# Optimization experiments

Hardware: AMD Instinct MI355X
Metric: run time of the kernel (lower is better)

## Reference

```python
import jax, jax.numpy as jnp
import numpy as np

B, S, HID = 1, 4096, 1024
NH, HD = 16, 64            # heads, per-head dim
BS = 256                    # block size
PB = 256                    # position buckets (= max_relative_positions)
EPS = 1e-7


def make_log_bucket_position(rel, num_buckets, max_position):
    sign = jnp.sign(rel)
    max_exact = num_buckets // 2
    in_exact = (rel < max_exact) & (rel > -max_exact)
    abs_pos = jnp.where(in_exact, max_exact - 1, jnp.abs(rel))
    x = jnp.log((max_position - 1) / max_exact)
    xx = jnp.log(abs_pos / max_exact) / x
    log_pos = jnp.ceil(xx * (max_exact - 1)) + max_exact
    return jnp.where(abs_pos <= max_exact, rel, (log_pos * sign).astype(jnp.int32)).astype(jnp.int32)


def split_into_blocks(x, block_size, axis):
    # [..., S, ...] -> [..., S//bs, bs, ...]; S assumed divisible by bs
    shp = x.shape
    new = shp[:axis] + (shp[axis] // block_size, block_size) + shp[axis + 1:]
    return x.reshape(new)


def concat_3_blocks(x, block_axis, seq_axis, pad_value=0):
    # pad one zero block on each side of the block axis, then concat
    # [prev, cur, next] along the within-block seq axis.
    pad = [(0, 0)] * x.ndim
    pad[block_axis] = (1, 1)
    xp = jnp.pad(x, pad, constant_values=pad_value)
    nb = x.shape[block_axis]
    slices = [jax.lax.dynamic_slice_in_dim(xp, i, nb, block_axis) for i in range(3)]
    return jnp.concatenate(slices, axis=seq_axis)


def layer_norm(x, scale, bias):
    mu = jnp.mean(x, axis=-1, keepdims=True)
    var = jnp.mean(jnp.square(x - mu), axis=-1, keepdims=True)
    return (x - mu) * jax.lax.rsqrt(var + EPS) * scale + bias


def setup_inputs() -> dict:
    key = jax.random.key(0)
    ks = jax.random.split(key, 8)
    d = {
        'hidden_states': jax.random.normal(ks[0], (B, S, HID), jnp.float32) * 0.02,
        'rel_pos_embeddings': jax.random.normal(ks[1], (S, HID), jnp.float32) * 0.02,
        'Wq': jax.random.normal(ks[2], (HID, HID), jnp.float32) * 0.01,
        'bq': jnp.zeros((HID,), jnp.float32),
        'Wk': jax.random.normal(ks[3], (HID, HID), jnp.float32) * 0.01,
        'bk': jnp.zeros((HID,), jnp.float32),
        'Wv': jax.random.normal(ks[4], (HID, HID), jnp.float32) * 0.01,
        'bv': jnp.zeros((HID,), jnp.float32),
        'Wo': jax.random.normal(ks[5], (HID, HID), jnp.float32) * 0.01,
        'bo': jnp.zeros((HID,), jnp.float32),
        'ln_scale': jnp.ones((HID,), jnp.float32),
        'ln_bias': jnp.zeros((HID,), jnp.float32),
    }
    return d


def reference(hidden_states, rel_pos_embeddings, Wq, bq, Wk, bk, Wv, bv, Wo, bo, ln_scale, ln_bias):
    b, s, hid = hidden_states.shape

    def heads(x):
        return x.reshape(x.shape[:-1] + (NH, HD))

    # content projections -> [B, nb, bs, h, d]
    q = split_into_blocks(heads(hidden_states @ Wq + bq), BS, axis=1)
    k = split_into_blocks(heads(hidden_states @ Wk + bk), BS, axis=1)
    v = split_into_blocks(heads(hidden_states @ Wv + bv), BS, axis=1)
    k3 = concat_3_blocks(k, block_axis=1, seq_axis=2)   # [B, nb, 3bs, h, d]
    v3 = concat_3_blocks(v, block_axis=1, seq_axis=2)

    c2c = jnp.einsum('bnqhd,bnkhd->bnhqk', q, k3)

    # position projections, stacked over batch (size-1 batch dim broadcasts in einsum)
    pos_q = split_into_blocks(heads(rel_pos_embeddings @ Wq + bq)[None], BS, axis=1)  # [1, nb, bs, h, d]
    pos_k = split_into_blocks(heads(rel_pos_embeddings @ Wk + bk)[None], BS, axis=1)
    pos_k3 = concat_3_blocks(pos_k, block_axis=1, seq_axis=2)                          # [1, nb, 3bs, h, d]

    rel = jnp.arange(BS, dtype=jnp.int32)[:, None] - jnp.arange(3 * BS, dtype=jnp.int32)[None, :]
    rel = make_log_bucket_position(rel, PB, PB)
    idx = jnp.clip(rel + PB, 0, 2 * PB - 1)            # [bs, 3bs]

    c2p = jnp.einsum('bnqhd,bnkhd->bnhqk', q, pos_k3)  # [B, nb, h, bs, 3bs]
    # faithful to the source: axis-less jnp.take gathers from the FLATTENED
    # score tensor -> [bs, 3bs] bias broadcast over (batch, block, head)
    c2p_bias = jnp.take(c2p, idx)

    p2c = jnp.einsum('bnqhd,bnkhd->bnhqk', pos_q, k3)
    p2c_bias = jnp.take(p2c, idx)

    scale = jnp.sqrt(jnp.asarray(HD * 3, hidden_states.dtype))
    attn = (c2c + c2p_bias + p2c_bias) / scale
    probs = jax.nn.softmax(attn, axis=-1)

    ctx = jnp.einsum('bnhqk,bnkhd->bnqhd', probs, v3)  # [B, nb, bs, h, d]
    ctx = ctx.reshape(b, s, hid)
    out = ctx @ Wo + bo
    return layer_norm(out + hidden_states, ln_scale, ln_bias)
```

## Files before the change

### kernel.cpp

```cpp
#include <hip/hip_runtime.h>
#include <stdint.h>

typedef unsigned short u16;
typedef __bf16 bf16_t;
typedef bf16_t v8bf __attribute__((ext_vector_type(8)));
typedef float v4f __attribute__((ext_vector_type(4)));

#define SEQ   4096
#define HIDN  1024
#define NHEAD 16
#define HDIM  64
#define BLK   256
#define NBLK  16

#define GLOAD_LDS16(g, l) __builtin_amdgcn_global_load_lds( \
  (const __attribute__((address_space(1))) unsigned*)(g), \
  (__attribute__((address_space(3))) unsigned*)(l), 16, 0, 0)

__device__ __forceinline__ u16 f2bf(float f){
  union { float f; unsigned u; } v; v.f = f;
  unsigned r = (v.u + 0x7fffu + ((v.u >> 16) & 1u)) >> 16;
  return (u16)r;
}
__device__ __forceinline__ float bf2f(u16 h){
  union { unsigned u; float f; } v; v.u = ((unsigned)h) << 16;
  return v.f;
}

__global__ __launch_bounds__(256) void k_prep(const float* __restrict__ hidden, u16* __restrict__ hb,
    const float* __restrict__ Wq, const float* __restrict__ Wk,
    const float* __restrict__ Wv, const float* __restrict__ Wo, u16* __restrict__ Wt,
    const float* __restrict__ bq, const float* __restrict__ bk, const float* __restrict__ bv,
    float* __restrict__ bcat,
    const float* __restrict__ rpe, float* __restrict__ posk, float* __restrict__ posq0)
{
  __shared__ float t[32][33];
  __shared__ float red[4][64];
  int b = blockIdx.x, tid = threadIdx.x;
  if (b < 4096){
    int w = b >> 10, tile = b & 1023;
    int k0 = (tile & 31) * 32, n0 = (tile >> 5) * 32;
    const float* W = (w == 0) ? Wq : (w == 1) ? Wk : (w == 2) ? Wv : Wo;
    u16* outp = Wt + (size_t)w * 1024 * 1024;
    int x = tid & 31, y = tid >> 5;
    #pragma unroll
    for (int yy = 0; yy < 32; yy += 8) t[y + yy][x] = W[(size_t)(k0 + y + yy) * 1024 + n0 + x];
    __syncthreads();
    #pragma unroll
    for (int yy = 0; yy < 32; yy += 8) outp[(size_t)(n0 + y + yy) * 1024 + k0 + x] = f2bf(t[x][y + yy]);
  } else if (b < 4608){
    int base = (b - 4096) * 8192;
    #pragma unroll
    for (int j = 0; j < 8; j++){
      int i = base + j * 1024 + tid * 4;
      float4 f = *(const float4*)&hidden[i];
      unsigned u0 = (unsigned)f2bf(f.x) | ((unsigned)f2bf(f.y) << 16);
      unsigned u1 = (unsigned)f2bf(f.z) | ((unsigned)f2bf(f.w) << 16);
      uint2 p; p.x = u0; p.y = u1;
      *(uint2*)&hb[i] = p;
    }
  } else if (b == 4608){
    #pragma unroll
    for (int j = 0; j < 12; j++){
      int i = j * 256 + tid;
      const float* src = i < 1024 ? bq : (i < 2048 ? bk : bv);
      bcat[i] = src[i & 1023];
    }
  } else {
    int pb = b - 4609;
    int d = tid & 63, part = tid >> 6;
    const float* W  = (pb < 256) ? Wk : Wq;
    const float* rv = (pb < 256) ? &rpe[(size_t)pb * 1024] : rpe;
    float s = 0.f;
    for (int k = part * 256; k < part * 256 + 256; k++) s += rv[k] * W[(size_t)k * 1024 + d];
    red[part][d] = s;
    __syncthreads();
    if (part == 0){
      s = red[0][d] + red[1][d] + red[2][d] + red[3][d];
      if (pb < 256) posk[pb * 64 + d] = s + bk[d];
      else          posq0[d] = s + bq[d];
    }
  }
}

__global__ __launch_bounds__(256) void k_gemm_qkv(const u16* __restrict__ A, const u16* __restrict__ Bt,
                                                  const float* __restrict__ bias,
                                                  u16* __restrict__ qk, u16* __restrict__ Vt)
{
  __shared__ alignas(16) u16 As[128 * 32];
  __shared__ alignas(16) u16 Bs[128 * 32];
  int tid = threadIdx.x, lane = tid & 63, wid = tid >> 6;
  int wr = wid >> 1, wc = wid & 1;
  int m0 = blockIdx.y * 128, n0 = blockIdx.x * 128;
  const int K = 1024;

  v4f acc[4][4];
  #pragma unroll
  for (int m = 0; m < 4; m++)
    #pragma unroll
    for (int n = 0; n < 4; n++) acc[m][n] = (v4f){0.f, 0.f, 0.f, 0.f};

  int r = lane & 15, g = lane >> 4;
  int ob0 = wid * 2048;

  for (int kt = 0; kt < K; kt += 32){
    #pragma unroll
    for (int t = 0; t < 2; ++t){
      int ob = ob0 + t * 1024;
      int o  = ob + lane * 16;
      int row = o >> 6, col = (o & 63) >> 1;
      GLOAD_LDS16(&A [(size_t)(m0 + row) * K + kt + col], As + (ob >> 1));
      GLOAD_LDS16(&Bt[(size_t)(n0 + row) * K + kt + col], Bs + (ob >> 1));
    }
    __syncthreads();
    v8bf a[4], bb[4];
    #pragma unroll
    for (int m = 0; m < 4; m++) a[m] = *(const v8bf*)&As[(wr * 64 + m * 16 + r) * 32 + g * 8];
    #pragma unroll
    for (int n = 0; n < 4; n++) bb[n] = *(const v8bf*)&Bs[(wc * 64 + n * 16 + r) * 32 + g * 8];
    #pragma unroll
    for (int m = 0; m < 4; m++)
      #pragma unroll
      for (int n = 0; n < 4; n++)
        acc[m][n] = __builtin_amdgcn_mfma_f32_16x16x32_bf16(a[m], bb[n], acc[m][n], 0, 0, 0);
    __syncthreads();
  }

  #pragma unroll
  for (int m = 0; m < 4; m++)
    #pragma unroll
    for (int n = 0; n < 4; n++){
      int col = n0 + wc * 64 + n * 16 + r;
      float bv = bias[col];
      #pragma unroll
      for (int i = 0; i < 4; i++){
        int row = m0 + wr * 64 + m * 16 + g * 4 + i;
        u16 h = f2bf(acc[m][n][i] + bv);
        if (col < 2048) qk[(size_t)row * 2048 + col] = h;
        else            Vt[(size_t)(col - 2048) * 4096 + row] = h;
      }
    }
}

__global__ __launch_bounds__(256) void k_gemm_out(const u16* __restrict__ A, const u16* __restrict__ Bt,
                                                  const float* __restrict__ bias,
                                                  const float* __restrict__ resid, float* __restrict__ Cout)
{
  __shared__ alignas(16) u16 As[128 * 32];
  __shared__ alignas(16) u16 Bs[128 * 32];
  int tid = threadIdx.x, lane = tid & 63, wid = tid >> 6;
  int wr = wid >> 1, wc = wid & 1;
  int m0 = blockIdx.y * 128, n0 = blockIdx.x * 128;
  const int K = 1024;

  v4f acc[4][4];
  #pragma unroll
  for (int m = 0; m < 4; m++)
    #pragma unroll
    for (int n = 0; n < 4; n++) acc[m][n] = (v4f){0.f, 0.f, 0.f, 0.f};

  int r = lane & 15, g = lane >> 4;
  int ob0 = wid * 2048;

  for (int kt = 0; kt < K; kt += 32){
    #pragma unroll
    for (int t = 0; t < 2; ++t){
      int ob = ob0 + t * 1024;
      int o  = ob + lane * 16;
      int row = o >> 6, col = (o & 63) >> 1;
      GLOAD_LDS16(&A [(size_t)(m0 + row) * K + kt + col], As + (ob >> 1));
      GLOAD_LDS16(&Bt[(size_t)(n0 + row) * K + kt + col], Bs + (ob >> 1));
    }
    __syncthreads();
    v8bf a[4], bb[4];
    #pragma unroll
    for (int m = 0; m < 4; m++) a[m] = *(const v8bf*)&As[(wr * 64 + m * 16 + r) * 32 + g * 8];
    #pragma unroll
    for (int n = 0; n < 4; n++) bb[n] = *(const v8bf*)&Bs[(wc * 64 + n * 16 + r) * 32 + g * 8];
    #pragma unroll
    for (int m = 0; m < 4; m++)
      #pragma unroll
      for (int n = 0; n < 4; n++)
        acc[m][n] = __builtin_amdgcn_mfma_f32_16x16x32_bf16(a[m], bb[n], acc[m][n], 0, 0, 0);
    __syncthreads();
  }

  #pragma unroll
  for (int m = 0; m < 4; m++)
    #pragma unroll
    for (int n = 0; n < 4; n++){
      int col = n0 + wc * 64 + n * 16 + r;
      float bv = bias[col];
      #pragma unroll
      for (int i = 0; i < 4; i++){
        int row = m0 + wr * 64 + m * 16 + g * 4 + i;
        Cout[(size_t)row * 1024 + col] = acc[m][n][i] + bv + resid[(size_t)row * 1024 + col];
      }
    }
}

__global__ __launch_bounds__(256) void k_brow(const u16* __restrict__ qk,
                                              const float* __restrict__ posk, const float* __restrict__ posq0,
                                              float* __restrict__ brow)
{
  int b = blockIdx.x, tid = threadIdx.x;
  if (tid < 32) brow[b * 32 + tid] = 0.f;
  int u = b * 32 + (tid >> 3), sub = tid & 7;
  float c2p = 0.f, p2c = 0.f;
  #pragma unroll
  for (int j = 0; j < 8; j++){
    int d = sub * 8 + j;
    c2p += bf2f(qk[d]) * posk[u * 64 + d];
    p2c += posq0[d] * bf2f(qk[(size_t)u * 2048 + 1024 + d]);
  }
  float v = c2p + p2c;
  v += __shfl_xor(v, 1);
  v += __shfl_xor(v, 2);
  v += __shfl_xor(v, 4);
  if (sub == 0) brow[256 + u] = v;
}

__global__ void k_biasd(const float* __restrict__ brow, float* __restrict__ biasd)
{
  int t = blockIdx.x * blockDim.x + threadIdx.x;
  int rel = t - 767;
  int bucket;
  bool in_exact = (rel < 128) && (rel > -128);
  int abs_pos = in_exact ? 127 : (rel < 0 ? -rel : rel);
  if (abs_pos <= 128) bucket = rel;
  else {
    float xx = logf((float)abs_pos * (1.0f / 128.0f)) / logf(255.0f / 128.0f);
    float lp = ceilf(xx * 127.0f) + 128.0f;
    int sgn = (rel > 0) ? 1 : ((rel < 0) ? -1 : 0);
    bucket = (int)lp * sgn;
  }
  int idx = bucket + 256;
  idx = idx < 0 ? 0 : (idx > 511 ? 511 : idx);
  biasd[t] = brow[idx];
}

__global__ __launch_bounds__(256) void k_attn(const u16* __restrict__ qk, const u16* __restrict__ Vt,
                                              const float* __restrict__ biasd, u16* __restrict__ ctxg)
{
  __shared__ alignas(16) u16 Qs[16 * 64];
  __shared__ alignas(16) u16 KVs[8192];
  __shared__ alignas(16) u16 Ss[16 * 776];
  __shared__ float bias_s[1024];
  __shared__ float wred[64];

  int b = blockIdx.x;
  int qt = b & 15, h = (b >> 4) & 15, n = b >> 8;
  int tid = threadIdx.x, lane = tid & 63, w = tid >> 6;
  int q0 = n * 256 + qt * 16;
  int qb0 = qt * 16;
  int g0 = (n - 1) * 256;
  const float c1 = 0.07216878364870323f * 1.4426950408889634f;

  int r = lane & 15, g = lane >> 4;

  if (w < 2){
    int o = w * 1024 + lane * 16;
    int row = o >> 7, p = (o >> 4) & 7;
    GLOAD_LDS16(&qk[(size_t)(q0 + row) * 2048 + h * 64 + ((p ^ (row & 7)) * 8)],
                ((u16*)Qs) + w * 512);
  }
  *(float4*)&bias_s[tid * 4] = *(const float4*)&biasd[tid * 4];

  float m4[4];
  #pragma unroll
  for (int i = 0; i < 4; i++) m4[i] = -3.0e38f;
  v4f sc[6][2];

  #pragma unroll
  for (int c = 0; c < 6; ++c){
    int cb = g0 + c * 128;
    bool oob = (cb < 0) || (cb >= SEQ);
    if (!oob){
      #pragma unroll
      for (int t = 0; t < 4; ++t){
        int o = (w * 4 + t) * 1024 + lane * 16;
        int row = o >> 7, p = (o >> 4) & 7;
        GLOAD_LDS16(&qk[(size_t)(cb + row) * 2048 + 1024 + h * 64 + ((p ^ (row & 7)) * 8)],
                    ((u16*)KVs) + (w * 4 + t) * 512);
      }
    }
    __syncthreads();
    v4f sacc[2];
    sacc[0] = (v4f){0.f,0.f,0.f,0.f};
    sacc[1] = (v4f){0.f,0.f,0.f,0.f};
    if (!oob){
      #pragma unroll
      for (int ks = 0; ks < 2; ++ks){
        v8bf a = *(const v8bf*)&Qs[r * 64 + ((4 * ks + g) ^ (r & 7)) * 8];
        #pragma unroll
        for (int nn = 0; nn < 2; nn++){
          int kr = w * 32 + nn * 16 + r;
          v8bf bb = *(const v8bf*)&KVs[kr * 64 + ((4 * ks + g) ^ (kr & 7)) * 8];
          sacc[nn] = __builtin_amdgcn_mfma_f32_16x16x32_bf16(a, bb, sacc[nn], 0, 0, 0);
        }
      }
    }
    #pragma unroll
    for (int nn = 0; nn < 2; nn++){
      int kcol = c * 128 + w * 32 + nn * 16 + r;
      #pragma unroll
      for (int i = 0; i < 4; i++){
        float s = (sacc[nn][i] + bias_s[qb0 + g * 4 + i - kcol + 767]) * c1;
        m4[i] = fmaxf(m4[i], s);
        sc[c][nn] [i] = s;
      }
    }
    __syncthreads();
  }

  #pragma unroll
  for (int i = 0; i < 4; i++){
    m4[i] = fmaxf(m4[i], __shfl_xor(m4[i], 1));
    m4[i] = fmaxf(m4[i], __shfl_xor(m4[i], 2));
    m4[i] = fmaxf(m4[i], __shfl_xor(m4[i], 4));
    m4[i] = fmaxf(m4[i], __shfl_xor(m4[i], 8));
  }
  if (r == 0){
    #pragma unroll
    for (int i = 0; i < 4; i++) wred[w * 16 + g * 4 + i] = m4[i];
  }
  __syncthreads();
  float mrow[4];
  #pragma unroll
  for (int i = 0; i < 4; i++){
    int row = g * 4 + i;
    mrow[i] = fmaxf(fmaxf(wred[row], wred[16 + row]), fmaxf(wred[32 + row], wred[48 + row]));
  }

  float s4[4] = {0.f, 0.f, 0.f, 0.f};
  #pragma unroll
  for (int c = 0; c < 6; ++c){
    #pragma unroll
    for (int nn = 0; nn < 2; nn++){
      int kcol = c * 128 + w * 32 + nn * 16 + r;
      int scol = kcol ^ (g << 4);
      #pragma unroll
      for (int i = 0; i < 4; i++){
        float p = exp2f(sc[c][nn][i] - mrow[i]);
        s4[i] += p;
        Ss[(g * 4 + i) * 776 + scol] = f2bf(p);
      }
    }
  }
  #pragma unroll
  for (int i = 0; i < 4; i++){
    s4[i] += __shfl_xor(s4[i], 1);
    s4[i] += __shfl_xor(s4[i], 2);
    s4[i] += __shfl_xor(s4[i], 4);
    s4[i] += __shfl_xor(s4[i], 8);
  }
  __syncthreads();
  if (r == 0){
    #pragma unroll
    for (int i = 0; i < 4; i++) wred[w * 16 + g * 4 + i] = s4[i];
  }
  __syncthreads();
  float inv4[4];
  #pragma unroll
  for (int i = 0; i < 4; i++){
    int row = g * 4 + i;
    inv4[i] = 1.0f / (wred[row] + wred[16 + row] + wred[32 + row] + wred[48 + row]);
  }

  v4f pacc = (v4f){0.f,0.f,0.f,0.f};
  int key = (r >> 2) & 3;
  for (int c = 0; c < 6; ++c){
    int cb = g0 + c * 128;
    bool oob = (cb < 0) || (cb >= SEQ);
    if (!oob){
      #pragma unroll
      for (int t = 0; t < 4; ++t){
        int o = (w * 4 + t) * 1024 + lane * 16;
        int d = o >> 8, p = (o >> 4) & 15;
        GLOAD_LDS16(&Vt[(size_t)(h * 64 + d) * 4096 + cb + ((p ^ (d & 7)) * 8)],
                    ((u16*)KVs) + (w * 4 + t) * 512);
      }
    }
    __syncthreads();
    if (!oob){
      int d = w * 16 + r;
      #pragma unroll
      for (int ks = 0; ks < 4; ++ks){
        int col = (c * 128 + ks * 32 + g * 8) ^ (key << 4);
        v8bf a  = *(const v8bf*)&Ss[r * 776 + col];
        v8bf bb = *(const v8bf*)&KVs[d * 128 + ((4 * ks + g) ^ (r & 7)) * 8];
        pacc = __builtin_amdgcn_mfma_f32_16x16x32_bf16(a, bb, pacc, 0, 0, 0);
      }
    }
    __syncthreads();
  }
  {
    int d = w * 16 + r;
    #pragma unroll
    for (int i = 0; i < 4; i++){
      int qrow = g * 4 + i;
      ctxg[(size_t)(q0 + qrow) * 1024 + h * 64 + d] = f2bf(pacc[i] * inv4[i]);
    }
  }
}

__global__ __launch_bounds__(256) void k_ln(float* __restrict__ out,
                                            const float* __restrict__ gamma, const float* __restrict__ beta)
{
  __shared__ float red[8];
  int row = blockIdx.x, tid = threadIdx.x;
  int lane = tid & 63, wid = tid >> 6;
  size_t base = (size_t)row * 1024 + tid * 4;
  float4 xv = *(const float4*)&out[base];
  float v0 = xv.x, v1 = xv.y, v2 = xv.z, v3 = xv.w;
  float s = v0 + v1 + v2 + v3;
  float q = v0 * v0 + v1 * v1 + v2 * v2 + v3 * v3;
  #pragma unroll
  for (int o = 32; o; o >>= 1){ s += __shfl_down(s, o); q += __shfl_down(q, o); }
  if (lane == 0){ red[wid] = s; red[4 + wid] = q; }
  __syncthreads();
  float ts = red[0] + red[1] + red[2] + red[3];
  float tq = red[4] + red[5] + red[6] + red[7];
  float mu = ts * (1.0f / 1024.0f);
  float var = tq * (1.0f / 1024.0f) - mu * mu;
  float rstd = rsqrtf(var + 1e-7f);
  int c = tid * 4;
  out[base + 0] = (v0 - mu) * rstd * gamma[c + 0] + beta[c + 0];
  out[base + 1] = (v1 - mu) * rstd * gamma[c + 1] + beta[c + 1];
  out[base + 2] = (v2 - mu) * rstd * gamma[c + 2] + beta[c + 2];
  out[base + 3] = (v3 - mu) * rstd * gamma[c + 3] + beta[c + 3];
}

extern "C" void kernel_launch(void* const* d_in, const int* in_sizes, int n_in,
                              void* d_out, int out_size, void* d_ws, size_t ws_size,
                              hipStream_t stream)
{
  const float* hidden = (const float*)d_in[0];
  const float* rpe    = (const float*)d_in[1];
  const float* Wq = (const float*)d_in[2];
  const float* bq = (const float*)d_in[3];
  const float* Wk = (const float*)d_in[4];
  const float* bk = (const float*)d_in[5];
  const float* Wv = (const float*)d_in[6];
  const float* bv = (const float*)d_in[7];
  const float* Wo = (const float*)d_in[8];
  const float* bo = (const float*)d_in[9];
  const float* lns = (const float*)d_in[10];
  const float* lnb = (const float*)d_in[11];
  float* out = (float*)d_out;

  char* ws = (char*)d_ws;
  size_t off = 0;
  auto alloc = [&](size_t bytes){ void* p = ws + off; off += (bytes + 255) & ~(size_t)255; return p; };
  u16* hb      = (u16*)alloc((size_t)SEQ * HIDN * 2);
  u16* Wt      = (u16*)alloc((size_t)4 * HIDN * HIDN * 2);
  u16* qk      = (u16*)alloc((size_t)SEQ * 2048 * 2);
  u16* Vt      = (u16*)alloc((size_t)HIDN * SEQ * 2);
  u16* ctxb    = (u16*)alloc((size_t)SEQ * HIDN * 2);
  float* bcat  = (float*)alloc(3072 * 4);
  float* poskf = (float*)alloc(256 * 64 * 4);
  float* posq0 = (float*)alloc(64 * 4);
  float* brow  = (float*)alloc(512 * 4);
  float* biasd = (float*)alloc(1024 * 4);
  (void)ws_size; (void)in_sizes; (void)n_in; (void)out_size;

  k_prep<<<4866, 256, 0, stream>>>(hidden, hb, Wq, Wk, Wv, Wo, Wt,
                                   bq, bk, bv, bcat, rpe, poskf, posq0);

  k_gemm_qkv<<<dim3(24, 32), 256, 0, stream>>>(hb, Wt, bcat, qk, Vt);

  k_brow<<<8, 256, 0, stream>>>(qk, poskf, posq0, brow);
  k_biasd<<<4, 256, 0, stream>>>(brow, biasd);

  k_attn<<<NBLK * NHEAD * 16, 256, 0, stream>>>(qk, Vt, biasd, ctxb);

  k_gemm_out<<<dim3(8, 32), 256, 0, stream>>>(ctxb, Wt + (size_t)3 * HIDN * HIDN, bo, hidden, out);

  k_ln<<<SEQ, 256, 0, stream>>>(out, lns, lnb);
}
```

Measured before the change: 172.6 us.

## Restructure block attention into online-softmax flash style with 64-query tiles

Rewrites the attention kernel so each workgroup handles 64 queries (16 per wave) instead of 16, loading K and V chunks together and accumulating P·V with an online softmax. This removes the two-pass structure, the cross-wave reductions and the second reload of K/V, and cuts the number of times K/V are fetched per query by a factor of four. In exchange the grid drops from 4096 to 1024 workgroups, which may lower occupancy and latency hiding, and the per-chunk rescaling adds some ALU work.

```diff
diff --git a/kernel.cpp b/kernel.cpp
--- a/kernel.cpp
+++ b/kernel.cpp
@@ -242,164 +242,143 @@
 __global__ __launch_bounds__(256) void k_attn(const u16* __restrict__ qk, const u16* __restrict__ Vt,
                                               const float* __restrict__ biasd, u16* __restrict__ ctxg)
 {
-  __shared__ alignas(16) u16 Qs[16 * 64];
-  __shared__ alignas(16) u16 KVs[8192];
-  __shared__ alignas(16) u16 Ss[16 * 776];
+  __shared__ alignas(16) u16 Ks[128 * 64];
+  __shared__ alignas(16) u16 Vs[64 * 128];
+  __shared__ alignas(16) u16 Ps[4 * 16 * 128];
   __shared__ float bias_s[1024];
-  __shared__ float wred[64];
 
   int b = blockIdx.x;
-  int qt = b & 15, h = (b >> 4) & 15, n = b >> 8;
+  int h = b & 15, tile = b >> 4;
+  int n = tile >> 2, qb0 = (tile & 3) * 64;
   int tid = threadIdx.x, lane = tid & 63, w = tid >> 6;
-  int q0 = n * 256 + qt * 16;
-  int qb0 = qt * 16;
+  int q0 = tile * 64;
   int g0 = (n - 1) * 256;
   const float c1 = 0.07216878364870323f * 1.4426950408889634f;
-
   int r = lane & 15, g = lane >> 4;
 
-  if (w < 2){
-    int o = w * 1024 + lane * 16;
-    int row = o >> 7, p = (o >> 4) & 7;
-    GLOAD_LDS16(&qk[(size_t)(q0 + row) * 2048 + h * 64 + ((p ^ (row & 7)) * 8)],
-                ((u16*)Qs) + w * 512);
-  }
   *(float4*)&bias_s[tid * 4] = *(const float4*)&biasd[tid * 4];
 
-  float m4[4];
-  #pragma unroll
-  for (int i = 0; i < 4; i++) m4[i] = -3.0e38f;
-  v4f sc[6][2];
-
-  #pragma unroll
+  v8bf qfrag[2];
+  {
+    const u16* src = &qk[(size_t)(q0 + w * 16 + r) * 2048 + h * 64 + g * 8];
+    qfrag[0] = *(const v8bf*)&src[0];
+    qfrag[1] = *(const v8bf*)&src[32];
+  }
+
+  u16* Pw = &Ps[w * 2048];
+  float m4[4], l4[4];
+  v4f pacc[4];
+  #pragma unroll
+  for (int i = 0; i < 4; i++){ m4[i] = -3.0e38f; l4[i] = 0.f; pacc[i] = (v4f){0.f,0.f,0.f,0.f}; }
+
   for (int c = 0; c < 6; ++c){
     int cb = g0 + c * 128;
     bool oob = (cb < 0) || (cb >= SEQ);
     if (!oob){
       #pragma unroll
       for (int t = 0; t < 4; ++t){
-        int o = (w * 4 + t) * 1024 + lane * 16;
-        int row = o >> 7, p = (o >> 4) & 7;
+        int row = w * 32 + t * 8 + (lane >> 3);
+        int p = lane & 7;
         GLOAD_LDS16(&qk[(size_t)(cb + row) * 2048 + 1024 + h * 64 + ((p ^ (row & 7)) * 8)],
-                    ((u16*)KVs) + (w * 4 + t) * 512);
-      }
-    }
-    __syncthreads();
-    v4f sacc[2];
-    sacc[0] = (v4f){0.f,0.f,0.f,0.f};
-    sacc[1] = (v4f){0.f,0.f,0.f,0.f};
+                    Ks + (size_t)(w * 32 + t * 8) * 64);
+      }
+      #pragma unroll
+      for (int t = 0; t < 4; ++t){
+        int d = w * 16 + t * 4 + (lane >> 4);
+        int p = lane & 15;
+        GLOAD_LDS16(&Vt[(size_t)(h * 64 + d) * 4096 + cb + ((p ^ (d & 7)) * 8)],
+                    Vs + (size_t)(w * 16 + t * 4) * 128);
+      }
+    }
+    __syncthreads();
+
+    v4f sacc[8];
+    #pragma unroll
+    for (int t = 0; t < 8; t++) sacc[t] = (v4f){0.f,0.f,0.f,0.f};
     if (!oob){
       #pragma unroll
       for (int ks = 0; ks < 2; ++ks){
-        v8bf a = *(const v8bf*)&Qs[r * 64 + ((4 * ks + g) ^ (r & 7)) * 8];
         #pragma unroll
-        for (int nn = 0; nn < 2; nn++){
-          int kr = w * 32 + nn * 16 + r;
-          v8bf bb = *(const v8bf*)&KVs[kr * 64 + ((4 * ks + g) ^ (kr & 7)) * 8];
-          sacc[nn] = __builtin_amdgcn_mfma_f32_16x16x32_bf16(a, bb, sacc[nn], 0, 0, 0);
+        for (int t = 0; t < 8; t++){
+          int kr = t * 16 + r;
+          v8bf bb = *(const v8bf*)&Ks[kr * 64 + (((4 * ks + g) ^ (kr & 7)) * 8)];
+          sacc[t] = __builtin_amdgcn_mfma_f32_16x16x32_bf16(qfrag[ks], bb, sacc[t], 0, 0, 0);
         }
       }
     }
-    #pragma unroll
-    for (int nn = 0; nn < 2; nn++){
-      int kcol = c * 128 + w * 32 + nn * 16 + r;
+
+    float sv[8][4];
+    float cm[4] = {-3.0e38f, -3.0e38f, -3.0e38f, -3.0e38f};
+    int ib = qb0 + g * 4 + 767 - r - c * 128;
+    #pragma unroll
+    for (int t = 0; t < 8; t++){
       #pragma unroll
       for (int i = 0; i < 4; i++){
-        float s = (sacc[nn][i] + bias_s[qb0 + g * 4 + i - kcol + 767]) * c1;
-        m4[i] = fmaxf(m4[i], s);
-        sc[c][nn] [i] = s;
-      }
-    }
-    __syncthreads();
-  }
-
+        float s = (sacc[t][i] + bias_s[ib + i - t * 16]) * c1;
+        sv[t][i] = s;
+        cm[i] = fmaxf(cm[i], s);
+      }
+    }
+    #pragma unroll
+    for (int i = 0; i < 4; i++){
+      cm[i] = fmaxf(cm[i], __shfl_xor(cm[i], 1));
+      cm[i] = fmaxf(cm[i], __shfl_xor(cm[i], 2));
+      cm[i] = fmaxf(cm[i], __shfl_xor(cm[i], 4));
+      cm[i] = fmaxf(cm[i], __shfl_xor(cm[i], 8));
+    }
+    #pragma unroll
+    for (int i = 0; i < 4; i++){
+      float mn = fmaxf(m4[i], cm[i]);
+      float sc = exp2f(m4[i] - mn);
+      m4[i] = mn;
+      l4[i] *= sc;
+      #pragma unroll
+      for (int nn = 0; nn < 4; nn++) pacc[nn][i] *= sc;
+    }
+    #pragma unroll
+    for (int t = 0; t < 8; t++){
+      #pragma unroll
+      for (int i = 0; i < 4; i++){
+        float p = exp2f(sv[t][i] - m4[i]);
+        l4[i] += p;
+        if (!oob){
+          int row = g * 4 + i;
+          Pw[row * 128 + (((2 * t + (r >> 3)) ^ (row & 7)) * 8) + (r & 7)] = f2bf(p);
+        }
+      }
+    }
+
+    if (!oob){
+      #pragma unroll
+      for (int ks = 0; ks < 4; ++ks){
+        v8bf a = *(const v8bf*)&Pw[r * 128 + (((4 * ks + g) ^ (r & 7)) * 8)];
+        #pragma unroll
+        for (int nn = 0; nn < 4; nn++){
+          int d = nn * 16 + r;
+          v8bf bb = *(const v8bf*)&Vs[d * 128 + (((4 * ks + g) ^ (d & 7)) * 8)];
+          pacc[nn] = __builtin_amdgcn_mfma_f32_16x16x32_bf16(a, bb, pacc[nn], 0, 0, 0);
+        }
+      }
+    }
+    __syncthreads();
+  }
+
+  float inv4[4];
   #pragma unroll
   for (int i = 0; i < 4; i++){
-    m4[i] = fmaxf(m4[i], __shfl_xor(m4[i], 1));
-    m4[i] = fmaxf(m4[i], __shfl_xor(m4[i], 2));
-    m4[i] = fmaxf(m4[i], __shfl_xor(m4[i], 4));
-    m4[i] = fmaxf(m4[i], __shfl_xor(m4[i], 8));
-  }
-  if (r == 0){
-    #pragma unroll
-    for (int i = 0; i < 4; i++) wred[w * 16 + g * 4 + i] = m4[i];
-  }
-  __syncthreads();
-  float mrow[4];
-  #pragma unroll
-  for (int i = 0; i < 4; i++){
-    int row = g * 4 + i;
-    mrow[i] = fmaxf(fmaxf(wred[row], wred[16 + row]), fmaxf(wred[32 + row], wred[48 + row]));
-  }
-
-  float s4[4] = {0.f, 0.f, 0.f, 0.f};
-  #pragma unroll
-  for (int c = 0; c < 6; ++c){
-    #pragma unroll
-    for (int nn = 0; nn < 2; nn++){
-      int kcol = c * 128 + w * 32 + nn * 16 + r;
-      int scol = kcol ^ (g << 4);
-      #pragma unroll
-      for (int i = 0; i < 4; i++){
-        float p = exp2f(sc[c][nn][i] - mrow[i]);
-        s4[i] += p;
-        Ss[(g * 4 + i) * 776 + scol] = f2bf(p);
-      }
-    }
-  }
-  #pragma unroll
-  for (int i = 0; i < 4; i++){
-    s4[i] += __shfl_xor(s4[i], 1);
-    s4[i] += __shfl_xor(s4[i], 2);
-    s4[i] += __shfl_xor(s4[i], 4);
-    s4[i] += __shfl_xor(s4[i], 8);
-  }
-  __syncthreads();
-  if (r == 0){
-    #pragma unroll
-    for (int i = 0; i < 4; i++) wred[w * 16 + g * 4 + i] = s4[i];
-  }
-  __syncthreads();
-  float inv4[4];
-  #pragma unroll
-  for (int i = 0; i < 4; i++){
-    int row = g * 4 + i;
-    inv4[i] = 1.0f / (wred[row] + wred[16 + row] + wred[32 + row] + wred[48 + row]);
-  }
-
-  v4f pacc = (v4f){0.f,0.f,0.f,0.f};
-  int key = (r >> 2) & 3;
-  for (int c = 0; c < 6; ++c){
-    int cb = g0 + c * 128;
-    bool oob = (cb < 0) || (cb >= SEQ);
-    if (!oob){
-      #pragma unroll
-      for (int t = 0; t < 4; ++t){
-        int o = (w * 4 + t) * 1024 + lane * 16;
-        int d = o >> 8, p = (o >> 4) & 15;
-        GLOAD_LDS16(&Vt[(size_t)(h * 64 + d) * 4096 + cb + ((p ^ (d & 7)) * 8)],
-                    ((u16*)KVs) + (w * 4 + t) * 512);
-      }
-    }
-    __syncthreads();
-    if (!oob){
-      int d = w * 16 + r;
-      #pragma unroll
-      for (int ks = 0; ks < 4; ++ks){
-        int col = (c * 128 + ks * 32 + g * 8) ^ (key << 4);
-        v8bf a  = *(const v8bf*)&Ss[r * 776 + col];
-        v8bf bb = *(const v8bf*)&KVs[d * 128 + ((4 * ks + g) ^ (r & 7)) * 8];
-        pacc = __builtin_amdgcn_mfma_f32_16x16x32_bf16(a, bb, pacc, 0, 0, 0);
-      }
-    }
-    __syncthreads();
-  }
-  {
-    int d = w * 16 + r;
+    l4[i] += __shfl_xor(l4[i], 1);
+    l4[i] += __shfl_xor(l4[i], 2);
+    l4[i] += __shfl_xor(l4[i], 4);
+    l4[i] += __shfl_xor(l4[i], 8);
+    inv4[i] = 1.0f / l4[i];
+  }
+  #pragma unroll
+  for (int nn = 0; nn < 4; nn++){
+    int d = nn * 16 + r;
     #pragma unroll
     for (int i = 0; i < 4; i++){
-      int qrow = g * 4 + i;
-      ctxg[(size_t)(q0 + qrow) * 1024 + h * 64 + d] = f2bf(pacc[i] * inv4[i]);
+      int qrow = q0 + w * 16 + g * 4 + i;
+      ctxg[(size_t)qrow * 1024 + h * 64 + d] = f2bf(pacc[nn][i] * inv4[i]);
     }
   }
 }
@@ -472,7 +451,7 @@
   k_brow<<<8, 256, 0, stream>>>(qk, poskf, posq0, brow);
   k_biasd<<<4, 256, 0, stream>>>(brow, biasd);
 
-  k_attn<<<NBLK * NHEAD * 16, 256, 0, stream>>>(qk, Vt, biasd, ctxb);
+  k_attn<<<64 * NHEAD, 256, 0, stream>>>(qk, Vt, biasd, ctxb);
 
   k_gemm_out<<<dim3(8, 32), 256, 0, stream>>>(ctxb, Wt + (size_t)3 * HIDN * HIDN, bo, hidden, out);
 
```

Result: faster. 151.8 us (-12.1%).
